# Kernel tuning notes

Hardware: AMD Instinct MI355X
Metric: run time of the kernel (lower is better)

The kernel has to match this reference:

```python
import jax, jax.numpy as jnp
import numpy as np

E = 1024      # embed_dim
H = 16        # num_heads
D = E // H    # head_dim = 64
K = 4         # num_hyper_nodes
MAX_SEQ = 8192
ROPE_BASE = 10000.0
SCALE = D ** -0.5


def rotate_half(x):
    half = x.shape[-1] // 2
    return jnp.concatenate([-x[..., half:], x[..., :half]], axis=-1)


def _rope_cache():
    inv_freq = 1.0 / (ROPE_BASE ** (jnp.arange(0, D, 2, dtype=jnp.float32) / D))
    t = jnp.arange(MAX_SEQ, dtype=jnp.float32)
    freqs = jnp.outer(t, inv_freq)                       # (MAX_SEQ, D/2)
    emb = jnp.concatenate([freqs, freqs], axis=-1)       # (MAX_SEQ, D)
    return jnp.cos(emb), jnp.sin(emb)


def setup_inputs() -> dict:
    key = jax.random.key(0)
    ks = jax.random.split(key, 6)
    B, S = 2, 2048
    w_scale = E ** -0.5  # keep pre-softmax logits in a sane range
    return {
        "x":  jax.random.normal(ks[0], (B, S, E), dtype=jnp.float32),
        "Wq": jax.random.normal(ks[1], (E, E), dtype=jnp.float32) * w_scale,
        "Wk": jax.random.normal(ks[2], (E, E), dtype=jnp.float32) * w_scale,
        "Wv": jax.random.normal(ks[3], (E, E), dtype=jnp.float32) * w_scale,
        "Wr": jax.random.normal(ks[4], (E, H * K), dtype=jnp.float32) * w_scale,
        "Wo": jax.random.normal(ks[5], (E, E), dtype=jnp.float32) * w_scale,
    }


def reference(x, Wq, Wk, Wv, Wr, Wo):
    B, S, _ = x.shape
    # projections -> (B, H, S, D)
    q = (x @ Wq).reshape(B, S, H, D).transpose(0, 2, 1, 3)
    k = (x @ Wk).reshape(B, S, H, D).transpose(0, 2, 1, 3)
    v = (x @ Wv).reshape(B, S, H, D).transpose(0, 2, 1, 3)

    # node routing probabilities (B, H, S, K)
    logits = (x @ Wr).reshape(B, S, H, K).transpose(0, 2, 1, 3)
    node_probs = jax.nn.softmax(logits, axis=-1)

    # expected per-node position: sum_{j<i} p[j,k]  -> (B, H, S, K)
    expected_pos = jnp.cumsum(node_probs, axis=2) - node_probs

    # fractional-position RoPE via linear interpolation of the cos/sin cache
    cos_c, sin_c = _rope_cache()
    pos = jnp.clip(expected_pos, 0.0, MAX_SEQ - 1)
    pf = pos.astype(jnp.int32)                   # floor
    pc = jnp.minimum(pf + 1, MAX_SEQ - 1)        # ceil
    frac = (pos - pf.astype(pos.dtype))[..., None]
    cos = cos_c[pf] + frac * (cos_c[pc] - cos_c[pf])   # (B,H,S,K,D)
    sin = sin_c[pf] + frac * (sin_c[pc] - sin_c[pf])

    # Weighted combine over nodes. Since q_k = q*cos_k + rh(q)*sin_k is linear
    # in (cos_k, sin_k), sum_k p_k * q_k = q * (sum_k p_k cos_k) + rh(q) * (sum_k p_k sin_k)
    cos_w = jnp.einsum('bhsk,bhskd->bhsd', node_probs, cos)
    sin_w = jnp.einsum('bhsk,bhskd->bhsd', node_probs, sin)
    q_r = q * cos_w + rotate_half(q) * sin_w
    k_r = k * cos_w + rotate_half(k) * sin_w

    # P(same node) weights (B, H, S, S)
    node_w = jnp.einsum('bhik,bhjk->bhij', node_probs, node_probs)

    scores = jnp.einsum('bhid,bhjd->bhij', q_r, k_r) * SCALE
    scores = scores + jnp.log(node_w + 1e-8)
    causal = jnp.tril(jnp.ones((S, S), dtype=bool))
    scores = jnp.where(causal[None, None], scores, -jnp.inf)
    attn = jax.nn.softmax(scores, axis=-1)

    out = jnp.einsum('bhij,bhjd->bhid', attn, v)
    out = out.transpose(0, 2, 1, 3).reshape(B, S, E)
    return out @ Wo
```

## Files before the change

### kernel.cpp

```cpp
#include <hip/hip_runtime.h>

#define E_ 1024
#define H_ 16
#define D_ 64
#define K_ 4
#define S_ 2048
#define B_ 2
#define BS_ 4096
#define BH_ 32
#define CT_ 2080

typedef __attribute__((ext_vector_type(8))) short short8;
typedef __attribute__((ext_vector_type(4))) float f32x4;
typedef __attribute__((ext_vector_type(4))) unsigned short u16x4;

__device__ __forceinline__ unsigned short f2bf(float f) {
  union { float f; unsigned u; } v; v.f = f;
  unsigned r = v.u + 0x7FFFu + ((v.u >> 16) & 1u);
  return (unsigned short)(r >> 16);
}
__device__ __forceinline__ float bf2f(unsigned short u) {
  union { unsigned u; float f; } v; v.u = ((unsigned)u) << 16; return v.f;
}

typedef __attribute__((address_space(1))) const void gvoid;
typedef __attribute__((address_space(3))) void lvoid;
__device__ __forceinline__ void gload_lds16(const void* g, void* l) {
  __builtin_amdgcn_global_load_lds((gvoid*)g, (lvoid*)l, 16, 0, 0);
}

__device__ __forceinline__ short8 lds8(const unsigned short* base, int row, int chunk) {
  int off = row * 128 + (((chunk ^ (row & 7)) & 7) << 4);
  return *(const short8*)((const char*)base + off);
}

#define SWZ_(d) (((d) & 7) ^ (((d) >> 3) & 7))

__global__ __launch_bounds__(256) void k_convert_x(const float* __restrict__ x,
                                                   unsigned short* __restrict__ xb) {
  int i = blockIdx.x * 256 + threadIdx.x;
  float4 v = ((const float4*)x)[i];
  u16x4 o; o.x = f2bf(v.x); o.y = f2bf(v.y); o.z = f2bf(v.z); o.w = f2bf(v.w);
  ((u16x4*)xb)[i] = o;
}

__global__ __launch_bounds__(256) void k_transpose_w(const float* __restrict__ Wq,
    const float* __restrict__ Wk, const float* __restrict__ Wv, const float* __restrict__ Wo,
    unsigned short* __restrict__ wt) {
  const float* W = blockIdx.z == 0 ? Wq : blockIdx.z == 1 ? Wk : blockIdx.z == 2 ? Wv : Wo;
  unsigned short* out = wt + (size_t)blockIdx.z * E_ * E_;
  __shared__ float tile[64][65];
  int k0 = blockIdx.y * 64, n0 = blockIdx.x * 64;
  int r = threadIdx.x >> 2, q4 = threadIdx.x & 3;
#pragma unroll
  for (int q = 0; q < 4; q++) {
    int c4 = q4 + q * 4;
    float4 v = *(const float4*)&W[(size_t)(k0 + r) * E_ + n0 + c4 * 4];
    tile[r][c4 * 4 + 0] = v.x; tile[r][c4 * 4 + 1] = v.y;
    tile[r][c4 * 4 + 2] = v.z; tile[r][c4 * 4 + 3] = v.w;
  }
  __syncthreads();
#pragma unroll
  for (int q = 0; q < 4; q++) {
    int cb = (q4 + q * 4) * 4;
    u16x4 o;
    o.x = f2bf(tile[cb + 0][r]); o.y = f2bf(tile[cb + 1][r]);
    o.z = f2bf(tile[cb + 2][r]); o.w = f2bf(tile[cb + 3][r]);
    *(u16x4*)&out[(size_t)(n0 + r) * E_ + k0 + cb] = o;
  }
}

__global__ __launch_bounds__(256) void k_cache(float* __restrict__ cosc, float* __restrict__ sinc) {
  int i = blockIdx.x * 256 + threadIdx.x;
  if (i >= CT_ * 32) return;
  int tt = i >> 5, f = i & 31;
  float invf = __expf(-(float)(2 * f) * (9.210340371976184f / 64.f));
  float ang = (float)tt * invf;
  cosc[i] = cosf(ang); sinc[i] = sinf(ang);
}

__global__ __launch_bounds__(256) void k_router(const float* __restrict__ x,
    const float* __restrict__ Wr, float* __restrict__ logits) {
  int rowblk = blockIdx.x * 8;
  int c = threadIdx.x & 63, rg = threadIdx.x >> 6;
  __shared__ float xs[8][128];
  float acc0 = 0.f, acc1 = 0.f;
  for (int e0 = 0; e0 < E_; e0 += 128) {
    __syncthreads();
    int idx = threadIdx.x;
    float4 v = *(const float4*)&x[(size_t)(rowblk + (idx >> 5)) * E_ + e0 + (idx & 31) * 4];
    *(float4*)&xs[idx >> 5][(idx & 31) * 4] = v;
    __syncthreads();
#pragma unroll 8
    for (int e = 0; e < 128; e++) {
      float w = Wr[(size_t)(e0 + e) * 64 + c];
      acc0 = fmaf(xs[rg * 2 + 0][e], w, acc0);
      acc1 = fmaf(xs[rg * 2 + 1][e], w, acc1);
    }
  }
  logits[(size_t)(rowblk + rg * 2 + 0) * 64 + c] = acc0;
  logits[(size_t)(rowblk + rg * 2 + 1) * 64 + c] = acc1;
}

__global__ __launch_bounds__(256) void k_scan(const float* __restrict__ logits,
    float* __restrict__ probs, unsigned short* __restrict__ pb, float* __restrict__ epos) {
  int bh = blockIdx.x; int b = bh >> 4, h = bh & 15;
  int t = threadIdx.x;
  float p[8][4];
  float own[4] = {0.f, 0.f, 0.f, 0.f};
#pragma unroll
  for (int r = 0; r < 8; r++) {
    int s = t * 8 + r;
    float4 lg = *(const float4*)&logits[(size_t)(b * S_ + s) * 64 + h * 4];
    float m = fmaxf(fmaxf(lg.x, lg.y), fmaxf(lg.z, lg.w));
    float e0 = __expf(lg.x - m), e1 = __expf(lg.y - m), e2 = __expf(lg.z - m), e3 = __expf(lg.w - m);
    float inv = 1.f / (e0 + e1 + e2 + e3);
    p[r][0] = e0 * inv; p[r][1] = e1 * inv; p[r][2] = e2 * inv; p[r][3] = e3 * inv;
    own[0] += p[r][0]; own[1] += p[r][1]; own[2] += p[r][2]; own[3] += p[r][3];
    float4 pv; pv.x = p[r][0]; pv.y = p[r][1]; pv.z = p[r][2]; pv.w = p[r][3];
    *(float4*)&probs[((size_t)bh * S_ + s) * 4] = pv;
    u16x4 pu; pu.x = f2bf(p[r][0]); pu.y = f2bf(p[r][1]);
    pu.z = f2bf(p[r][2]); pu.w = f2bf(p[r][3]);
    *(u16x4*)&pb[((size_t)bh * S_ + s) * 4] = pu;
  }
  __shared__ float sc[4][256];
#pragma unroll
  for (int k = 0; k < 4; k++) sc[k][t] = own[k];
  __syncthreads();
  for (int off = 1; off < 256; off <<= 1) {
    float v0 = 0, v1 = 0, v2 = 0, v3 = 0;
    if (t >= off) { v0 = sc[0][t - off]; v1 = sc[1][t - off]; v2 = sc[2][t - off]; v3 = sc[3][t - off]; }
    __syncthreads();
    if (t >= off) { sc[0][t] += v0; sc[1][t] += v1; sc[2][t] += v2; sc[3][t] += v3; }
    __syncthreads();
  }
  float run[4];
#pragma unroll
  for (int k = 0; k < 4; k++) run[k] = sc[k][t] - own[k];
#pragma unroll
  for (int r = 0; r < 8; r++) {
    int s = t * 8 + r;
    float4 ev; ev.x = run[0]; ev.y = run[1]; ev.z = run[2]; ev.w = run[3];
    *(float4*)&epos[((size_t)bh * S_ + s) * 4] = ev;
    run[0] += p[r][0]; run[1] += p[r][1]; run[2] += p[r][2]; run[3] += p[r][3];
  }
}

__global__ __launch_bounds__(256) void k_cwsw(const float* __restrict__ probs,
    const float* __restrict__ epos, const float* __restrict__ cosc, const float* __restrict__ sinc,
    float* __restrict__ cw, float* __restrict__ sw) {
  int bh = blockIdx.y;
  int s = blockIdx.x * 8 + (threadIdx.x >> 5);
  int f = threadIdx.x & 31;
  size_t row = (size_t)bh * S_ + s;
  float cacc = 0.f, sacc = 0.f;
#pragma unroll
  for (int k = 0; k < 4; k++) {
    float pk = probs[row * 4 + k];
    float pos = epos[row * 4 + k];
    pos = fminf(fmaxf(pos, 0.f), (float)(CT_ - 2));
    int pf = (int)pos; float fr = pos - (float)pf;
    float c0 = cosc[pf * 32 + f], c1 = cosc[pf * 32 + 32 + f];
    float s0 = sinc[pf * 32 + f], s1 = sinc[pf * 32 + 32 + f];
    cacc = fmaf(pk, c0 + fr * (c1 - c0), cacc);
    sacc = fmaf(pk, s0 + fr * (s1 - s0), sacc);
  }
  cw[row * 32 + f] = cacc; sw[row * 32 + f] = sacc;
}

__device__ __forceinline__ void gemm_128x128(const unsigned short* __restrict__ A,
    const unsigned short* __restrict__ Bt, int m0, int n0,
    unsigned short* lA, unsigned short* lB, f32x4 acc[4][4]) {
  int t = threadIdx.x, w = t >> 6, lane = t & 63;
  int wm = w >> 1, wn = w & 1;
  int arow = lane & 15, agrp = lane >> 4;
  for (int k0 = 0; k0 < E_; k0 += 64) {
    __syncthreads();
#pragma unroll
    for (int j = 0; j < 4; j++) {
      int c = j * 256 + w * 64 + lane;
      int row = c >> 3, slot = c & 7;
      gload_lds16(A + (size_t)(m0 + row) * E_ + k0 + ((slot ^ (row & 7)) << 3),
                  lA + (size_t)(j * 256 + w * 64) * 8);
      gload_lds16(Bt + (size_t)(n0 + row) * E_ + k0 + ((slot ^ (row & 7)) << 3),
                  lB + (size_t)(j * 256 + w * 64) * 8);
    }
    __syncthreads();
#pragma unroll
    for (int ks = 0; ks < 2; ks++) {
      short8 af[4], bfr[4];
#pragma unroll
      for (int mi = 0; mi < 4; mi++) af[mi] = lds8(lA, wm * 64 + mi * 16 + arow, ks * 4 + agrp);
#pragma unroll
      for (int nj = 0; nj < 4; nj++) bfr[nj] = lds8(lB, wn * 64 + nj * 16 + arow, ks * 4 + agrp);
#pragma unroll
      for (int mi = 0; mi < 4; mi++)
#pragma unroll
        for (int nj = 0; nj < 4; nj++)
          acc[mi][nj] = __builtin_amdgcn_mfma_f32_16x16x32_bf16(af[mi], bfr[nj], acc[mi][nj], 0, 0, 0);
    }
  }
}

__global__ __launch_bounds__(256) void k_gemm_qkv(const unsigned short* __restrict__ xb,
    const unsigned short* __restrict__ wt, const float* __restrict__ cw, const float* __restrict__ sw,
    unsigned short* __restrict__ qr, unsigned short* __restrict__ kr, unsigned short* __restrict__ vb) {
  __shared__ unsigned short lA[128 * 64], lB[128 * 64];
  int z = blockIdx.z;
  int m0 = blockIdx.y * 128, n0 = blockIdx.x * 128;
  f32x4 acc[4][4];
  f32x4 zero4 = {0.f, 0.f, 0.f, 0.f};
#pragma unroll
  for (int a = 0; a < 4; a++)
#pragma unroll
    for (int b2 = 0; b2 < 4; b2++) acc[a][b2] = zero4;
  gemm_128x128(xb, wt + (size_t)z * E_ * E_, m0, n0, lA, lB, acc);

  int t = threadIdx.x, w = t >> 6, lane = t & 63;
  int wm = w >> 1, wn = w & 1;
  int arow = lane & 15, agrp = lane >> 4;
  if (z == 2) {
#pragma unroll
    for (int mi = 0; mi < 4; mi++)
#pragma unroll
      for (int reg = 0; reg < 4; reg++) {
        int i = m0 + wm * 64 + mi * 16 + agrp * 4 + reg;
        int b = i >> 11, s = i & 2047;
#pragma unroll
        for (int nj = 0; nj < 4; nj++) {
          int col = n0 + wn * 64 + nj * 16 + arow;
          int h = col >> 6, d = col & 63;
          vb[((size_t)(b * H_ + h) * S_ + s) * 64 + d] = f2bf(acc[mi][nj][reg]);
        }
      }
  } else {
    unsigned short* out = (z == 0) ? qr : kr;
    float scl = (z == 0) ? 0.18033688011f : 1.0f;
    int h = (n0 + wn * 64) >> 6;
#pragma unroll
    for (int mi = 0; mi < 4; mi++)
#pragma unroll
      for (int reg = 0; reg < 4; reg++) {
        int i = m0 + wm * 64 + mi * 16 + agrp * 4 + reg;
        int b = i >> 11, s = i & 2047;
        size_t rbase = (size_t)(b * H_ + h) * S_ + s;
        float cw0 = cw[rbase * 32 + arow], cw1 = cw[rbase * 32 + 16 + arow];
        float sw0 = sw[rbase * 32 + arow], sw1 = sw[rbase * 32 + 16 + arow];
#pragma unroll
        for (int nj = 0; nj < 4; nj++) {
          float v = acc[mi][nj][reg];
          float part = acc[mi][nj ^ 2][reg];
          float rh = (nj < 2) ? -part : part;
          float cwv = (nj & 1) ? cw1 : cw0;
          float swv = (nj & 1) ? sw1 : sw0;
          out[rbase * 64 + nj * 16 + arow] = f2bf((v * cwv + rh * swv) * scl);
        }
      }
  }
}

__global__ __launch_bounds__(256) void k_gemm_out(const unsigned short* __restrict__ ob,
    const unsigned short* __restrict__ wot, float* __restrict__ dout) {
  __shared__ unsigned short lA[64 * 64];
  __shared__ unsigned short lB[128 * 64];
  int m0 = blockIdx.y * 64, n0 = blockIdx.x * 128;
  int t = threadIdx.x, w = t >> 6, lane = t & 63;
  int arow = lane & 15, agrp = lane >> 4;
  f32x4 acc[4][2];
  f32x4 zero4 = {0.f, 0.f, 0.f, 0.f};
#pragma unroll
  for (int a = 0; a < 4; a++) { acc[a][0] = zero4; acc[a][1] = zero4; }
  for (int k0 = 0; k0 < E_; k0 += 64) {
    __syncthreads();
#pragma unroll
    for (int j = 0; j < 2; j++) {
      int c = j * 256 + t;
      int row = c >> 3, slot = c & 7;
      gload_lds16(ob + (size_t)(m0 + row) * E_ + k0 + ((slot ^ (row & 7)) << 3),
                  lA + (size_t)c * 8);
    }
#pragma unroll
    for (int j = 0; j < 4; j++) {
      int c = j * 256 + t;
      int row = c >> 3, slot = c & 7;
      gload_lds16(wot + (size_t)(n0 + row) * E_ + k0 + ((slot ^ (row & 7)) << 3),
                  lB + (size_t)c * 8);
    }
    __syncthreads();
#pragma unroll
    for (int ks = 0; ks < 2; ks++) {
      short8 af[4], bfr[2];
#pragma unroll
      for (int mi = 0; mi < 4; mi++) af[mi] = lds8(lA, mi * 16 + arow, ks * 4 + agrp);
#pragma unroll
      for (int nj = 0; nj < 2; nj++) bfr[nj] = lds8(lB, w * 32 + nj * 16 + arow, ks * 4 + agrp);
#pragma unroll
      for (int mi = 0; mi < 4; mi++)
#pragma unroll
        for (int nj = 0; nj < 2; nj++)
          acc[mi][nj] = __builtin_amdgcn_mfma_f32_16x16x32_bf16(af[mi], bfr[nj], acc[mi][nj], 0, 0, 0);
    }
  }
#pragma unroll
  for (int mi = 0; mi < 4; mi++)
#pragma unroll
    for (int reg = 0; reg < 4; reg++) {
      int i = m0 + mi * 16 + agrp * 4 + reg;
#pragma unroll
      for (int nj = 0; nj < 2; nj++) {
        int col = n0 + w * 32 + nj * 16 + arow;
        dout[(size_t)i * E_ + col] = acc[mi][nj][reg];
      }
    }
}

__device__ const int4 kChunk[38] = {
  { 8,0, 8, 8},{ 8,9,17, 9},{12,0, 8,19},{12,9,17,20},
  { 7,0, 7, 6},{ 7,8,15, 7},{10,0, 7,13},{11,0, 7,16},{11,8,15,17},{11,16,23,18},
  {12,18,25,21},{14,0, 7,26},{14,8,15,27},{15,0, 7,30},{15,8,15,31},{15,16,23,32},
  {15,24,31,33},{ 3,0, 7,-1},
  { 6,0, 6, 4},{ 6,7,13, 5},{ 9,0, 6,10},{ 9,7,13,11},{10,8,14,14},{10,15,21,15},
  {13,0, 6,22},{13,7,13,23},{13,14,20,24},{13,21,27,25},{14,16,22,28},{14,23,29,29},
  { 5,0, 5, 2},{ 5,6,11, 3},{ 9,14,19,12},{ 2,0, 5,-1},
  { 4,0, 4, 0},{ 4,5, 9, 1},{ 1,0, 3,-1},{ 0,0, 1,-1}
};

__device__ __forceinline__ void qk_phase(const unsigned short* lKc, const short8 qf[2][2],
                                         int arow, int agrp, f32x4 sacc[2][4]) {
#pragma unroll
  for (int ks = 0; ks < 2; ks++)
#pragma unroll
    for (int ct = 0; ct < 4; ct++) {
      short8 kf = lds8(lKc, ct * 16 + arow, ks * 4 + agrp);
      sacc[0][ct] = __builtin_amdgcn_mfma_f32_16x16x32_bf16(qf[0][ks], kf, sacc[0][ct], 0, 0, 0);
      sacc[1][ct] = __builtin_amdgcn_mfma_f32_16x16x32_bf16(qf[1][ks], kf, sacc[1][ct], 0, 0, 0);
    }
}

__device__ __forceinline__ void softmax_half(const f32x4 sacc[4], const short8 piF,
    const short8 pjF[4], unsigned short* lPh, int kv0, int ig_base, int arow, int agrp,
    float mrow[4], float lrow[4], f32x4 oacc[4]) {
  f32x4 eps4 = {1e-8f, 1e-8f, 1e-8f, 1e-8f};
  f32x4 nwa[4];
#pragma unroll
  for (int ct = 0; ct < 4; ct++)
    nwa[ct] = __builtin_amdgcn_mfma_f32_16x16x32_bf16(piF, pjF[ct], eps4, 0, 0, 0);
  float sv[4][4];
  float rmax[4] = {-1e30f, -1e30f, -1e30f, -1e30f};
  if (kv0 + 63 > ig_base) {
#pragma unroll
    for (int ct = 0; ct < 4; ct++) {
      int jg = kv0 + ct * 16 + arow;
#pragma unroll
      for (int reg = 0; reg < 4; reg++) {
        int ig = ig_base + agrp * 4 + reg;
        float xv = sacc[ct][reg];
        if (jg > ig) xv = -1e30f;
        sv[ct][reg] = xv;
        rmax[reg] = fmaxf(rmax[reg], xv);
      }
    }
  } else {
#pragma unroll
    for (int ct = 0; ct < 4; ct++)
#pragma unroll
      for (int reg = 0; reg < 4; reg++) {
        float xv = sacc[ct][reg];
        sv[ct][reg] = xv;
        rmax[reg] = fmaxf(rmax[reg], xv);
      }
  }
#pragma unroll
  for (int reg = 0; reg < 4; reg++) {
    rmax[reg] = fmaxf(rmax[reg], __shfl_xor(rmax[reg], 1, 16));
    rmax[reg] = fmaxf(rmax[reg], __shfl_xor(rmax[reg], 2, 16));
    rmax[reg] = fmaxf(rmax[reg], __shfl_xor(rmax[reg], 4, 16));
    rmax[reg] = fmaxf(rmax[reg], __shfl_xor(rmax[reg], 8, 16));
  }
  float alpha[4], rsum[4];
#pragma unroll
  for (int reg = 0; reg < 4; reg++) {
    float mn = fmaxf(mrow[reg], rmax[reg]);
    alpha[reg] = __builtin_amdgcn_exp2f(mrow[reg] - mn);
    mrow[reg] = mn; rsum[reg] = 0.f;
  }
#pragma unroll
  for (int ct = 0; ct < 4; ct++)
#pragma unroll
    for (int reg = 0; reg < 4; reg++) {
      float p = __builtin_amdgcn_exp2f(sv[ct][reg] - mrow[reg]) * nwa[ct][reg];
      sv[ct][reg] = p; rsum[reg] += p;
    }
#pragma unroll
  for (int reg = 0; reg < 4; reg++) {
    rsum[reg] += __shfl_xor(rsum[reg], 1, 16);
    rsum[reg] += __shfl_xor(rsum[reg], 2, 16);
    rsum[reg] += __shfl_xor(rsum[reg], 4, 16);
    rsum[reg] += __shfl_xor(rsum[reg], 8, 16);
    lrow[reg] = lrow[reg] * alpha[reg] + rsum[reg];
  }
#pragma unroll
  for (int dt = 0; dt < 4; dt++) {
    f32x4 o = oacc[dt];
    o.x *= alpha[0]; o.y *= alpha[1]; o.z *= alpha[2]; o.w *= alpha[3];
    oacc[dt] = o;
  }
#pragma unroll
  for (int ct = 0; ct < 4; ct++)
#pragma unroll
    for (int reg = 0; reg < 4; reg++) {
      int row = agrp * 4 + reg, col = ct * 16 + arow;
      int off = row * 128 + ((col * 2) ^ ((row & 7) << 4));
      *(unsigned short*)((char*)lPh + off) = f2bf(sv[ct][reg]);
    }
}

__device__ __forceinline__ void pv_phase(const unsigned short* lP0, const unsigned short* lP1,
    const unsigned short* lVc, int arow, int agrp, f32x4 oacc0[4], f32x4 oacc1[4]) {
#pragma unroll
  for (int ks = 0; ks < 2; ks++) {
    short8 pf0 = lds8(lP0, arow, ks * 4 + agrp);
    short8 pf1 = lds8(lP1, arow, ks * 4 + agrp);
#pragma unroll
    for (int dt = 0; dt < 4; dt++) {
      int d = dt * 16 + arow;
      int off = d * 128 + ((((ks * 4 + agrp)) ^ SWZ_(d)) << 4);
      short8 vf = *(const short8*)((const char*)lVc + off);
      oacc0[dt] = __builtin_amdgcn_mfma_f32_16x16x32_bf16(pf0, vf, oacc0[dt], 0, 0, 0);
      oacc1[dt] = __builtin_amdgcn_mfma_f32_16x16x32_bf16(pf1, vf, oacc1[dt], 0, 0, 0);
    }
  }
}

__global__ __launch_bounds__(256, 2) void k_attn(const unsigned short* __restrict__ qr,
    const unsigned short* __restrict__ kr, const unsigned short* __restrict__ vb,
    const unsigned short* __restrict__ pb, unsigned short* __restrict__ ob,
    unsigned short* __restrict__ ObP, float* __restrict__ ml) {
  __shared__ unsigned short lK[2][64 * 64];
  __shared__ unsigned short lV[2][64 * 64];
  __shared__ unsigned short lP[4][2][16 * 64];
  int id = blockIdx.x;
  int xcd = id & 7, slt = id >> 3;
  int bh = xcd * 4 + (slt & 3);
  int4 ck = kChunk[slt >> 2];
  int qt2 = ck.x, j0 = ck.y, j1 = ck.z, part = ck.w;
  int t = threadIdx.x, w = t >> 6, lane = t & 63;
  int arow = lane & 15, agrp = lane >> 4;
  int q0 = qt2 * 128;
  size_t base = (size_t)bh * S_ * 64;
  size_t bhS = (size_t)bh * S_;

  short8 qf[2][2];
  short8 piF[2];
  float mrow[2][4], lrow[2][4];
  f32x4 oacc[2][4];
  f32x4 zero4 = {0.f, 0.f, 0.f, 0.f};
#pragma unroll
  for (int hh = 0; hh < 2; hh++) {
#pragma unroll
    for (int ks = 0; ks < 2; ks++)
      qf[hh][ks] = *(const short8*)&qr[base + (size_t)(q0 + hh * 64 + w * 16 + arow) * 64 + ks * 32 + agrp * 8];
    u16x4 pv = {0, 0, 0, 0};
    if (agrp == 0) pv = *(const u16x4*)&pb[(bhS + q0 + hh * 64 + w * 16 + arow) * 4];
    short8 z = {0, 0, 0, 0, 0, 0, 0, 0};
    z[0] = (short)pv.x; z[1] = (short)pv.y; z[2] = (short)pv.z; z[3] = (short)pv.w;
    piF[hh] = z;
#pragma unroll
    for (int reg = 0; reg < 4; reg++) { mrow[hh][reg] = -1e30f; lrow[hh][reg] = 0.f; }
#pragma unroll
    for (int dt = 0; dt < 4; dt++) oacc[hh][dt] = zero4;
  }

  auto stageK = [&](int jt, int buf) {
#pragma unroll
    for (int j = 0; j < 2; j++) {
      int c = j * 256 + w * 64 + lane;
      int row = c >> 3, slot = c & 7;
      gload_lds16(kr + base + (size_t)(jt * 64 + row) * 64 + ((slot ^ (row & 7)) << 3),
                  &lK[buf][(size_t)(j * 256 + w * 64) * 8]);
    }
  };
  auto loadV = [&](int jt, short8 vr[2]) {
#pragma unroll
    for (int j = 0; j < 2; j++) {
      int c = j * 256 + t;
      int row = c >> 3, d0 = (c & 7) * 8;
      vr[j] = *(const short8*)&vb[base + (size_t)(jt * 64 + row) * 64 + d0];
    }
  };
  auto scatterV = [&](const short8 vr[2], int buf) {
#pragma unroll
    for (int j = 0; j < 2; j++) {
      int c = j * 256 + t;
      int row = c >> 3, d0 = (c & 7) * 8;
#pragma unroll
      for (int x = 0; x < 8; x++) {
        int d = d0 + x;
        int off = d * 128 + ((row * 2) ^ (SWZ_(d) << 4));
        *(unsigned short*)((char*)&lV[buf][0] + off) = (unsigned short)vr[j][x];
      }
    }
  };
  auto loadPj = [&](int jt, u16x4 pj[4]) {
#pragma unroll
    for (int ct = 0; ct < 4; ct++) {
      u16x4 z = {0, 0, 0, 0};
      if (agrp == 0) z = *(const u16x4*)&pb[(bhS + jt * 64 + ct * 16 + arow) * 4];
      pj[ct] = z;
    }
  };

  short8 vreg[2];
  u16x4 pjv[4], pjvn[4];
  loadV(j0, vreg);
  stageK(j0, 0);
  scatterV(vreg, 0);
  loadPj(j0, pjv);
  __syncthreads();

  int nt = j1 - j0 + 1;
  for (int i = 0; i < nt; i++) {
    int cur = i & 1;
    int kv0 = (j0 + i) * 64;
    bool hn = (i + 1) < nt;
    if (hn) {
      loadV(j0 + i + 1, vreg);
      stageK(j0 + i + 1, cur ^ 1);
    }

    f32x4 sacc[2][4];
#pragma unroll
    for (int hh = 0; hh < 2; hh++)
#pragma unroll
      for (int ct = 0; ct < 4; ct++) sacc[hh][ct] = zero4;

    __builtin_amdgcn_s_setprio(1);
    qk_phase(&lK[cur][0], qf, arow, agrp, sacc);
    __builtin_amdgcn_s_setprio(0);

    short8 pjF[4];
#pragma unroll
    for (int ct = 0; ct < 4; ct++) {
      short8 z = {0, 0, 0, 0, 0, 0, 0, 0};
      z[0] = (short)pjv[ct].x; z[1] = (short)pjv[ct].y;
      z[2] = (short)pjv[ct].z; z[3] = (short)pjv[ct].w;
      pjF[ct] = z;
    }
#pragma unroll
    for (int hh = 0; hh < 2; hh++)
      softmax_half(sacc[hh], piF[hh], pjF, &lP[w][hh][0], kv0, q0 + hh * 64 + w * 16,
                   arow, agrp, mrow[hh], lrow[hh], oacc[hh]);

    if (hn) {
      scatterV(vreg, cur ^ 1);
      loadPj(j0 + i + 1, pjvn);
    }

    asm volatile("s_waitcnt lgkmcnt(0)" ::: "memory");
    __builtin_amdgcn_sched_barrier(0);
    __builtin_amdgcn_s_setprio(1);
    pv_phase(&lP[w][0][0], &lP[w][1][0], &lV[cur][0], arow, agrp, oacc[0], oacc[1]);
    __builtin_amdgcn_s_setprio(0);
    if (hn) {
#pragma unroll
      for (int ct = 0; ct < 4; ct++) pjv[ct] = pjvn[ct];
    }
    __syncthreads();
  }

  if (part >= 0) {
    unsigned short* Op = ObP + ((size_t)bh * 34 + part) * 8192;
    float* mlp = ml + ((size_t)bh * 34 + part) * 256;
#pragma unroll
    for (int hh = 0; hh < 2; hh++) {
#pragma unroll
      for (int dt = 0; dt < 4; dt++)
#pragma unroll
        for (int reg = 0; reg < 4; reg++) {
          int row = hh * 64 + w * 16 + agrp * 4 + reg;
          Op[row * 64 + dt * 16 + arow] = f2bf(oacc[hh][dt][reg]);
        }
      if (arow == 0) {
#pragma unroll
        for (int reg = 0; reg < 4; reg++) {
          int row = hh * 64 + w * 16 + agrp * 4 + reg;
          mlp[row] = mrow[hh][reg];
          mlp[128 + row] = lrow[hh][reg];
        }
      }
    }
  } else {
    int b = bh >> 4, h8 = bh & 15;
#pragma unroll
    for (int hh = 0; hh < 2; hh++)
#pragma unroll
      for (int dt = 0; dt < 4; dt++)
#pragma unroll
        for (int reg = 0; reg < 4; reg++) {
          int i = q0 + hh * 64 + w * 16 + agrp * 4 + reg;
          int d = dt * 16 + arow;
          float v = oacc[hh][dt][reg] / lrow[hh][reg];
          ob[((size_t)(b * S_ + i) * H_ + h8) * 64 + d] = f2bf(v);
        }
  }
}

__global__ __launch_bounds__(256) void k_merge(const unsigned short* __restrict__ ObP,
    const float* __restrict__ ml, unsigned short* __restrict__ ob) {
  int qx = blockIdx.x, bh = blockIdx.y;
  int qt2 = 4 + qx;
  int np = qt2 <= 8 ? 2 : (qt2 <= 12 ? 3 : 4);
  int bslot = qt2 <= 8 ? (qt2 - 4) * 2 : (qt2 <= 12 ? 10 + (qt2 - 9) * 3 : 22 + (qt2 - 13) * 4);
  int t = threadIdx.x;
  int r = t >> 1, dh = (t & 1) * 32;
  float mp[4], lp[4];
  float m = -1e30f;
  for (int p2 = 0; p2 < np; p2++) {
    const float* mlp = ml + ((size_t)bh * 34 + bslot + p2) * 256;
    mp[p2] = mlp[r]; lp[p2] = mlp[128 + r];
    m = fmaxf(m, mp[p2]);
  }
  float a[4], l = 0.f;
  for (int p2 = 0; p2 < np; p2++) { a[p2] = __builtin_amdgcn_exp2f(mp[p2] - m); l = fmaf(lp[p2], a[p2], l); }
  float inv = 1.f / l;
  for (int p2 = 0; p2 < np; p2++) a[p2] *= inv;
  int i = qt2 * 128 + r, b = bh >> 4, h = bh & 15;
  unsigned short* op = ob + ((size_t)(b * S_ + i) * H_ + h) * 64 + dh;
#pragma unroll
  for (int q = 0; q < 8; q++) {
    float a0 = 0.f, a1 = 0.f, a2 = 0.f, a3 = 0.f;
    for (int p2 = 0; p2 < np; p2++) {
      const unsigned short* Op = ObP + ((size_t)bh * 34 + bslot + p2) * 8192 + r * 64 + dh + q * 4;
      u16x4 xx = *(const u16x4*)Op;
      a0 = fmaf(bf2f(xx.x), a[p2], a0);
      a1 = fmaf(bf2f(xx.y), a[p2], a1);
      a2 = fmaf(bf2f(xx.z), a[p2], a2);
      a3 = fmaf(bf2f(xx.w), a[p2], a3);
    }
    u16x4 o; o.x = f2bf(a0); o.y = f2bf(a1); o.z = f2bf(a2); o.w = f2bf(a3);
    *(u16x4*)(op + q * 4) = o;
  }
}

extern "C" void kernel_launch(void* const* d_in, const int* in_sizes, int n_in,
                              void* d_out, int out_size, void* d_ws, size_t ws_size,
                              hipStream_t stream) {
  const float* x  = (const float*)d_in[0];
  const float* Wq = (const float*)d_in[1];
  const float* Wk = (const float*)d_in[2];
  const float* Wv = (const float*)d_in[3];
  const float* Wr = (const float*)d_in[4];
  const float* Wo = (const float*)d_in[5];
  float* dout = (float*)d_out;

  char* p = (char*)d_ws;
  auto alloc = [&](size_t bytes) -> char* {
    char* r = p; p += (bytes + 255) & ~(size_t)255; return r;
  };
  unsigned short* xb   = (unsigned short*)alloc((size_t)BS_ * E_ * 2);
  unsigned short* wt   = (unsigned short*)alloc((size_t)4 * E_ * E_ * 2);
  float* cosc          = (float*)alloc((size_t)CT_ * 32 * 4);
  float* sinc          = (float*)alloc((size_t)CT_ * 32 * 4);
  float* probs         = (float*)alloc((size_t)BH_ * S_ * 4 * 4);
  unsigned short* pb   = (unsigned short*)alloc((size_t)BH_ * S_ * 4 * 2);
  float* logits        = (float*)alloc((size_t)BS_ * 64 * 4);
  float* epos          = (float*)alloc((size_t)BH_ * S_ * 4 * 4);
  float* cw            = (float*)alloc((size_t)BH_ * S_ * 32 * 4);
  float* sw            = (float*)alloc((size_t)BH_ * S_ * 32 * 4);
  unsigned short* qrb  = (unsigned short*)alloc((size_t)BH_ * S_ * 64 * 2);
  unsigned short* krb  = (unsigned short*)alloc((size_t)BH_ * S_ * 64 * 2);
  unsigned short* vbb  = (unsigned short*)alloc((size_t)BH_ * S_ * 64 * 2);
  unsigned short* obb  = (unsigned short*)alloc((size_t)BS_ * E_ * 2);
  if ((size_t)(p - (char*)d_ws) > ws_size) return;

  unsigned short* ObP = (unsigned short*)logits;
  float* mlbuf = (float*)xb;

  k_convert_x<<<BS_ * E_ / 4 / 256, 256, 0, stream>>>(x, xb);
  k_transpose_w<<<dim3(16, 16, 4), 256, 0, stream>>>(Wq, Wk, Wv, Wo, wt);
  k_cache<<<(CT_ * 32 + 255) / 256, 256, 0, stream>>>(cosc, sinc);
  k_router<<<BS_ / 8, 256, 0, stream>>>(x, Wr, logits);
  k_scan<<<BH_, 256, 0, stream>>>(logits, probs, pb, epos);
  k_cwsw<<<dim3(S_ / 8, BH_), 256, 0, stream>>>(probs, epos, cosc, sinc, cw, sw);
  k_gemm_qkv<<<dim3(8, 32, 3), 256, 0, stream>>>(xb, wt, cw, sw, qrb, krb, vbb);
  k_attn<<<dim3(38 * BH_), 256, 0, stream>>>(qrb, krb, vbb, pb, obb, ObP, mlbuf);
  k_merge<<<dim3(12, BH_), 256, 0, stream>>>(ObP, mlbuf, obb);
  k_gemm_out<<<dim3(8, 64), 256, 0, stream>>>(obb, wt + (size_t)3 * E_ * E_, dout);
}
```

Measured before the change: 224.1 us.

## Compute softmax row sums via MFMA, lazy rescale, and DPP max reductions

Drops the shuffle-based row-sum reduction and gets the softmax denominator from an extra MFMA of P against a ones vector, run alongside the PV product. The online-softmax rescale of the accumulators is skipped whenever no row max has grown by more than a threshold, so exp values stay bounded. The first two steps of the max reduction use DPP instead of ds_swizzle shuffles, and the final normalisation multiplies by a reciprocal instead of dividing. The trade-offs are two extra MFMAs per tile, a wave-wide vote branch, and a denominator built from the bf16-rounded P rather than the fp32 values.

```diff
diff --git a/kernel.cpp b/kernel.cpp
--- a/kernel.cpp
+++ b/kernel.cpp
@@ -35,6 +35,16 @@
 }
 
 #define SWZ_(d) (((d) & 7) ^ (((d) >> 3) & 7))
+
+__device__ __forceinline__ float redmax16(float v) {
+  int iv = __float_as_int(v);
+  v = fmaxf(v, __int_as_float(__builtin_amdgcn_update_dpp(iv, iv, 0xB1, 0xF, 0xF, true)));
+  iv = __float_as_int(v);
+  v = fmaxf(v, __int_as_float(__builtin_amdgcn_update_dpp(iv, iv, 0x4E, 0xF, 0xF, true)));
+  v = fmaxf(v, __shfl_xor(v, 4, 16));
+  v = fmaxf(v, __shfl_xor(v, 8, 16));
+  return v;
+}
 
 __global__ __launch_bounds__(256) void k_convert_x(const float* __restrict__ x,
                                                    unsigned short* __restrict__ xb) {
@@ -339,7 +349,7 @@
 
 __device__ __forceinline__ void softmax_half(const f32x4 sacc[4], const short8 piF,
     const short8 pjF[4], unsigned short* lPh, int kv0, int ig_base, int arow, int agrp,
-    float mrow[4], float lrow[4], f32x4 oacc[4]) {
+    float mrow[4], f32x4 oacc[4], f32x4& o4) {
   f32x4 eps4 = {1e-8f, 1e-8f, 1e-8f, 1e-8f};
   f32x4 nwa[4];
 #pragma unroll
@@ -371,56 +381,46 @@
       }
   }
 #pragma unroll
-  for (int reg = 0; reg < 4; reg++) {
-    rmax[reg] = fmaxf(rmax[reg], __shfl_xor(rmax[reg], 1, 16));
-    rmax[reg] = fmaxf(rmax[reg], __shfl_xor(rmax[reg], 2, 16));
-    rmax[reg] = fmaxf(rmax[reg], __shfl_xor(rmax[reg], 4, 16));
-    rmax[reg] = fmaxf(rmax[reg], __shfl_xor(rmax[reg], 8, 16));
-  }
-  float alpha[4], rsum[4];
-#pragma unroll
-  for (int reg = 0; reg < 4; reg++) {
-    float mn = fmaxf(mrow[reg], rmax[reg]);
-    alpha[reg] = __builtin_amdgcn_exp2f(mrow[reg] - mn);
-    mrow[reg] = mn; rsum[reg] = 0.f;
+  for (int reg = 0; reg < 4; reg++) rmax[reg] = redmax16(rmax[reg]);
+  bool ok = (rmax[0] <= mrow[0] + 11.5f) & (rmax[1] <= mrow[1] + 11.5f) &
+            (rmax[2] <= mrow[2] + 11.5f) & (rmax[3] <= mrow[3] + 11.5f);
+  if (!__all(ok)) {
+    float alpha[4];
+#pragma unroll
+    for (int reg = 0; reg < 4; reg++) {
+      float mn = fmaxf(mrow[reg], rmax[reg]);
+      alpha[reg] = __builtin_amdgcn_exp2f(mrow[reg] - mn);
+      mrow[reg] = mn;
+    }
+#pragma unroll
+    for (int dt = 0; dt < 4; dt++) {
+      f32x4 o = oacc[dt];
+      o.x *= alpha[0]; o.y *= alpha[1]; o.z *= alpha[2]; o.w *= alpha[3];
+      oacc[dt] = o;
+    }
+    o4.x *= alpha[0]; o4.y *= alpha[1]; o4.z *= alpha[2]; o4.w *= alpha[3];
   }
 #pragma unroll
   for (int ct = 0; ct < 4; ct++)
 #pragma unroll
     for (int reg = 0; reg < 4; reg++) {
       float p = __builtin_amdgcn_exp2f(sv[ct][reg] - mrow[reg]) * nwa[ct][reg];
-      sv[ct][reg] = p; rsum[reg] += p;
-    }
-#pragma unroll
-  for (int reg = 0; reg < 4; reg++) {
-    rsum[reg] += __shfl_xor(rsum[reg], 1, 16);
-    rsum[reg] += __shfl_xor(rsum[reg], 2, 16);
-    rsum[reg] += __shfl_xor(rsum[reg], 4, 16);
-    rsum[reg] += __shfl_xor(rsum[reg], 8, 16);
-    lrow[reg] = lrow[reg] * alpha[reg] + rsum[reg];
-  }
-#pragma unroll
-  for (int dt = 0; dt < 4; dt++) {
-    f32x4 o = oacc[dt];
-    o.x *= alpha[0]; o.y *= alpha[1]; o.z *= alpha[2]; o.w *= alpha[3];
-    oacc[dt] = o;
-  }
-#pragma unroll
-  for (int ct = 0; ct < 4; ct++)
-#pragma unroll
-    for (int reg = 0; reg < 4; reg++) {
       int row = agrp * 4 + reg, col = ct * 16 + arow;
       int off = row * 128 + ((col * 2) ^ ((row & 7) << 4));
-      *(unsigned short*)((char*)lPh + off) = f2bf(sv[ct][reg]);
+      *(unsigned short*)((char*)lPh + off) = f2bf(p);
     }
 }
 
 __device__ __forceinline__ void pv_phase(const unsigned short* lP0, const unsigned short* lP1,
-    const unsigned short* lVc, int arow, int agrp, f32x4 oacc0[4], f32x4 oacc1[4]) {
+    const unsigned short* lVc, int arow, int agrp, f32x4 oacc0[4], f32x4 oacc1[4],
+    f32x4& o40, f32x4& o41) {
+  const short8 ones = {16256, 16256, 16256, 16256, 16256, 16256, 16256, 16256};
 #pragma unroll
   for (int ks = 0; ks < 2; ks++) {
     short8 pf0 = lds8(lP0, arow, ks * 4 + agrp);
     short8 pf1 = lds8(lP1, arow, ks * 4 + agrp);
+    o40 = __builtin_amdgcn_mfma_f32_16x16x32_bf16(pf0, ones, o40, 0, 0, 0);
+    o41 = __builtin_amdgcn_mfma_f32_16x16x32_bf16(pf1, ones, o41, 0, 0, 0);
 #pragma unroll
     for (int dt = 0; dt < 4; dt++) {
       int d = dt * 16 + arow;
@@ -452,8 +452,9 @@
 
   short8 qf[2][2];
   short8 piF[2];
-  float mrow[2][4], lrow[2][4];
+  float mrow[2][4];
   f32x4 oacc[2][4];
+  f32x4 o4[2];
   f32x4 zero4 = {0.f, 0.f, 0.f, 0.f};
 #pragma unroll
   for (int hh = 0; hh < 2; hh++) {
@@ -466,9 +467,10 @@
     z[0] = (short)pv.x; z[1] = (short)pv.y; z[2] = (short)pv.z; z[3] = (short)pv.w;
     piF[hh] = z;
 #pragma unroll
-    for (int reg = 0; reg < 4; reg++) { mrow[hh][reg] = -1e30f; lrow[hh][reg] = 0.f; }
+    for (int reg = 0; reg < 4; reg++) mrow[hh][reg] = -1e30f;
 #pragma unroll
     for (int dt = 0; dt < 4; dt++) oacc[hh][dt] = zero4;
+    o4[hh] = zero4;
   }
 
   auto stageK = [&](int jt, int buf) {
@@ -549,7 +551,7 @@
 #pragma unroll
     for (int hh = 0; hh < 2; hh++)
       softmax_half(sacc[hh], piF[hh], pjF, &lP[w][hh][0], kv0, q0 + hh * 64 + w * 16,
-                   arow, agrp, mrow[hh], lrow[hh], oacc[hh]);
+                   arow, agrp, mrow[hh], oacc[hh], o4[hh]);
 
     if (hn) {
       scatterV(vreg, cur ^ 1);
@@ -559,7 +561,8 @@
     asm volatile("s_waitcnt lgkmcnt(0)" ::: "memory");
     __builtin_amdgcn_sched_barrier(0);
     __builtin_amdgcn_s_setprio(1);
-    pv_phase(&lP[w][0][0], &lP[w][1][0], &lV[cur][0], arow, agrp, oacc[0], oacc[1]);
+    pv_phase(&lP[w][0][0], &lP[w][1][0], &lV[cur][0], arow, agrp, oacc[0], oacc[1],
+             o4[0], o4[1]);
     __builtin_amdgcn_s_setprio(0);
     if (hn) {
 #pragma unroll
@@ -585,23 +588,27 @@
         for (int reg = 0; reg < 4; reg++) {
           int row = hh * 64 + w * 16 + agrp * 4 + reg;
           mlp[row] = mrow[hh][reg];
-          mlp[128 + row] = lrow[hh][reg];
+          mlp[128 + row] = o4[hh][reg];
         }
       }
     }
   } else {
     int b = bh >> 4, h8 = bh & 15;
 #pragma unroll
-    for (int hh = 0; hh < 2; hh++)
+    for (int hh = 0; hh < 2; hh++) {
+      f32x4 inv4;
+      inv4.x = 1.f / o4[hh].x; inv4.y = 1.f / o4[hh].y;
+      inv4.z = 1.f / o4[hh].z; inv4.w = 1.f / o4[hh].w;
 #pragma unroll
       for (int dt = 0; dt < 4; dt++)
 #pragma unroll
         for (int reg = 0; reg < 4; reg++) {
           int i = q0 + hh * 64 + w * 16 + agrp * 4 + reg;
           int d = dt * 16 + arow;
-          float v = oacc[hh][dt][reg] / lrow[hh][reg];
+          float v = oacc[hh][dt][reg] * inv4[reg];
           ob[((size_t)(b * S_ + i) * H_ + h8) * 64 + d] = f2bf(v);
         }
+    }
   }
 }
 
```

Measured after the change: 210.8 us. 1.06x faster.
